# Performance work log

Hardware: AMD Instinct MI355X
Metric: run time of the kernel (lower is better)

Reference implementation:

```python
import jax, jax.numpy as jnp
import numpy as np

N_NODES = 50000
N_EDGES = 800000
F_IN = 128
HID = 256


def setup_inputs() -> dict:
    key = jax.random.key(0)
    ks = jax.random.split(key, 10)
    x = jax.random.normal(ks[0], (N_NODES, F_IN), jnp.float32)
    edge_index = jax.random.randint(ks[1], (2, N_EDGES), 0, N_NODES, jnp.int32)
    # Glorot-ish scaled weights (PyG Linear default init style)
    def w(k, o, i):
        return jax.random.normal(k, (o, i), jnp.float32) * (1.0 / np.sqrt(i))
    return {
        "x": x,
        "edge_index": edge_index,
        "W1l": w(ks[2], HID, F_IN), "b1l": jnp.zeros((HID,), jnp.float32),
        "W1r": w(ks[3], HID, F_IN),
        "W2l": w(ks[4], HID, HID), "b2l": jnp.zeros((HID,), jnp.float32),
        "W2r": w(ks[5], HID, HID),
        "Wh1": w(ks[6], 4, HID), "bh1": jnp.zeros((4,), jnp.float32),
        "Wh2": w(ks[7], 3, HID), "bh2": jnp.zeros((3,), jnp.float32),
    }


def sage_conv(x, edge_index, Wl, bl, Wr):
    # PyG SAGEConv (aggr='mean'): out_i = Wl @ mean_{j in N(i)} x_j + bl + Wr @ x_i
    src, dst = edge_index[0], edge_index[1]
    n = x.shape[0]
    summed = jax.ops.segment_sum(x[src], dst, num_segments=n)        # [N, F]
    cnt = jax.ops.segment_sum(jnp.ones((src.shape[0],), x.dtype), dst, num_segments=n)
    agg = summed / jnp.maximum(cnt, 1.0)[:, None]                    # isolated nodes -> 0
    return agg @ Wl.T + bl + x @ Wr.T


def reference(x, edge_index, W1l, b1l, W1r, W2l, b2l, W2r, Wh1, bh1, Wh2, bh2):
    h = jax.nn.relu(sage_conv(x, edge_index, W1l, b1l, W1r))
    # dropout(p=0.5) is identity in eval mode
    h = sage_conv(h, edge_index, W2l, b2l, W2r)
    out1 = h @ Wh1.T + bh1   # l2_classifier=False branch
    out2 = h @ Wh2.T + bh2
    return (out1, out2, h)
```

## Files before the change

kernel.cpp:

```cpp
#include <hip/hip_runtime.h>
#include <hip/hip_bf16.h>

typedef short bf16x8 __attribute__((ext_vector_type(8)));
typedef float f32x4 __attribute__((ext_vector_type(4)));

__device__ __forceinline__ float bf2f(__hip_bfloat16 v) { return __bfloat162float(v); }
__device__ __forceinline__ float sh2f(short s) {
    union { float f; unsigned u; } c; c.u = ((unsigned)(unsigned short)s) << 16; return c.f;
}
__device__ __forceinline__ short f2sh(float f) {
    __hip_bfloat16 b = __float2bfloat16(f); return *(short*)&b;
}

__device__ __forceinline__ float loadAny(const void* p, size_t i, int isf32) {
    return isf32 ? ((const float*)p)[i] : bf2f(((const __hip_bfloat16*)p)[i]);
}

__global__ void pre_kernel(const void* __restrict__ x,
                           const void* W1l, const void* W1r, const void* W2l, const void* W2r,
                           const void* b1l, const void* b2l, const void* Wh1, const void* Wh2,
                           const void* bh1, const void* bh2,
                           __hip_bfloat16* __restrict__ xn,
                           __hip_bfloat16* __restrict__ W1c, __hip_bfloat16* __restrict__ W2c,
                           __hip_bfloat16* __restrict__ sb,
                           int* __restrict__ deg, int* __restrict__ flag, int N) {
    __shared__ int sflag;
    int tid = threadIdx.x;
    if (tid < 64) {
        const unsigned short* xu = (const unsigned short*)x;
        unsigned short u = xu[tid * 2];
        unsigned e = (u >> 7) & 0xFF;
        bool good = (u == 0) || (e >= 110 && e <= 137);
        unsigned long long m = __ballot(good);
        if (tid == 0) sflag = (__popcll(m) < 32) ? 1 : 0;
    }
    __syncthreads();
    int isf32 = sflag;
    int gid = blockIdx.x * 256 + tid;
    if (gid == 0) *flag = isf32;
    if (gid < N) deg[gid] = 0;

    int n4 = N * 32;
    if (gid < n4) {
        short4 o;
        if (isf32) {
            float4 v = ((const float4*)x)[gid];
            o.x = f2sh(v.x); o.y = f2sh(v.y); o.z = f2sh(v.z); o.w = f2sh(v.w);
        } else {
            o = ((const short4*)x)[gid];
        }
        ((short4*)xn)[gid] = o;
    }

    if (gid < 65536) {
        int n = gid >> 8, k = gid & 255;
        float v = (k < 128) ? loadAny(W1l, n * 128 + k, isf32)
                            : loadAny(W1r, n * 128 + (k - 128), isf32);
        W1c[gid] = __float2bfloat16(v);
        return;
    }
    int u = gid - 65536;
    if (u < 131072) {
        int n = u >> 9, k = u & 511;
        float v = (k < 256) ? loadAny(W2l, n * 256 + k, isf32)
                            : loadAny(W2r, n * 256 + (k - 256), isf32);
        W2c[u] = __float2bfloat16(v);
        return;
    }
    int s = u - 131072;
    float v;
    if      (s < 256)  v = loadAny(b1l, s, isf32);
    else if (s < 512)  v = loadAny(b2l, s - 256, isf32);
    else if (s < 1536) v = loadAny(Wh1, s - 512, isf32);
    else if (s < 2304) v = loadAny(Wh2, s - 1536, isf32);
    else if (s < 2308) v = loadAny(bh1, s - 2304, isf32);
    else if (s < 2311) v = loadAny(bh2, s - 2308, isf32);
    else return;
    sb[s] = __float2bfloat16(v);
}

__global__ void deg_kernel(const int* __restrict__ ei, int E, int* __restrict__ deg,
                           int* __restrict__ rank) {
    int t = blockIdx.x * blockDim.x + threadIdx.x;
    if (t >= E) return;
    rank[t] = atomicAdd(&deg[ei[E + t]], 1);
}

__global__ __launch_bounds__(256) void scanA_kernel(const int* __restrict__ deg,
                                                    int* __restrict__ off,
                                                    int* __restrict__ bsum, int N) {
    __shared__ int ts[256];
    int t = threadIdx.x;
    int base = blockIdx.x * 1024 + t * 4;
    int v0 = (base + 0 < N) ? deg[base + 0] : 0;
    int v1 = (base + 1 < N) ? deg[base + 1] : 0;
    int v2 = (base + 2 < N) ? deg[base + 2] : 0;
    int v3 = (base + 3 < N) ? deg[base + 3] : 0;
    int i0 = v0, i1 = i0 + v1, i2 = i1 + v2, i3 = i2 + v3;
    ts[t] = i3;
    __syncthreads();
    for (int d = 1; d < 256; d <<= 1) {
        int x = (t >= d) ? ts[t - d] : 0;
        __syncthreads();
        ts[t] += x;
        __syncthreads();
    }
    int excl = (t > 0) ? ts[t - 1] : 0;
    if (base + 0 < N) off[base + 1] = excl + i0;
    if (base + 1 < N) off[base + 2] = excl + i1;
    if (base + 2 < N) off[base + 3] = excl + i2;
    if (base + 3 < N) off[base + 4] = excl + i3;
    if (t == 255) bsum[blockIdx.x] = ts[255];
}

__global__ void addC_kernel(int* __restrict__ off, const int* __restrict__ bsum,
                            int N, int nb) {
    __shared__ int ex[64];
    int t = threadIdx.x;
    if (t < 64) {
        int v = (t < nb) ? bsum[t] : 0;
        for (int d = 1; d < 64; d <<= 1) {
            int y = __shfl_up(v, d, 64);
            if (t >= d) v += y;
        }
        ex[t] = v;
    }
    __syncthreads();
    int i = blockIdx.x * 256 + t;
    if (i == 0) off[0] = 0;
    if (i < N) {
        int b = i >> 10;
        int excl = (b > 0) ? ex[b - 1] : 0;
        off[i + 1] += excl;
    }
}

__global__ void fill_kernel(const int* __restrict__ ei, int E,
                            const int* __restrict__ off, const int* __restrict__ rank,
                            unsigned short* __restrict__ srcs) {
    int t = blockIdx.x * blockDim.x + threadIdx.x;
    if (t >= E) return;
    int dst = ei[E + t];
    int pos = off[dst] + rank[t];
    srcs[pos] = (unsigned short)ei[t];
}

__global__ void gather1_kernel(const __hip_bfloat16* __restrict__ x,
                               const int* __restrict__ off,
                               const unsigned short* __restrict__ srcs,
                               __hip_bfloat16* __restrict__ agg, int N) {
    int gid  = blockIdx.x * blockDim.x + threadIdx.x;
    int wid  = gid >> 6;
    int lane = threadIdx.x & 63;
    int node = wid * 4 + (lane >> 4);
    int t    = lane & 15;
    if (node >= N) return;
    int beg = off[node], end = off[node + 1];
    float a[8] = {0.f, 0.f, 0.f, 0.f, 0.f, 0.f, 0.f, 0.f};
    const bf16x8* xb = (const bf16x8*)x;
    int e = beg;
    for (; e + 7 < end; e += 8) {
        bf16x8 v[8];
#pragma unroll
        for (int j = 0; j < 8; j++) v[j] = xb[(size_t)srcs[e + j] * 16 + t];
#pragma unroll
        for (int j = 0; j < 8; j++)
#pragma unroll
            for (int k = 0; k < 8; k++) a[k] += sh2f(v[j][k]);
    }
    for (; e < end; e++) {
        bf16x8 v = xb[(size_t)srcs[e] * 16 + t];
#pragma unroll
        for (int k = 0; k < 8; k++) a[k] += sh2f(v[k]);
    }
    float inv = 1.0f / fmaxf((float)(end - beg), 1.0f);
    bf16x8 o;
#pragma unroll
    for (int k = 0; k < 8; k++) o[k] = f2sh(a[k] * inv);
    ((bf16x8*)agg)[(size_t)node * 16 + t] = o;
}

__global__ void gather2_kernel(const __hip_bfloat16* __restrict__ h,
                               const int* __restrict__ off,
                               const unsigned short* __restrict__ srcs,
                               __hip_bfloat16* __restrict__ agg, int N) {
    int gid  = blockIdx.x * blockDim.x + threadIdx.x;
    int wid  = gid >> 6;
    int lane = threadIdx.x & 63;
    int node = wid * 2 + (lane >> 5);
    int t    = lane & 31;
    if (node >= N) return;
    int beg = off[node], end = off[node + 1];
    float a[8] = {0.f, 0.f, 0.f, 0.f, 0.f, 0.f, 0.f, 0.f};
    const bf16x8* hb = (const bf16x8*)h;
    int e = beg;
    for (; e + 7 < end; e += 8) {
        bf16x8 v[8];
#pragma unroll
        for (int j = 0; j < 8; j++) v[j] = hb[(size_t)srcs[e + j] * 32 + t];
#pragma unroll
        for (int j = 0; j < 8; j++)
#pragma unroll
            for (int k = 0; k < 8; k++) a[k] += sh2f(v[j][k]);
    }
    for (; e < end; e++) {
        bf16x8 v = hb[(size_t)srcs[e] * 32 + t];
#pragma unroll
        for (int k = 0; k < 8; k++) a[k] += sh2f(v[k]);
    }
    float inv = 1.0f / fmaxf((float)(end - beg), 1.0f);
    bf16x8 o;
#pragma unroll
    for (int k = 0; k < 8; k++) o[k] = f2sh(a[k] * inv);
    ((bf16x8*)agg)[(size_t)node * 32 + t] = o;
}

struct AFrag { bf16x8 v[2]; };

template <int K, int KA, bool RELU, bool TOOUT>
__global__ __launch_bounds__(256) void gemm_lds(const __hip_bfloat16* __restrict__ A1,
                                                const __hip_bfloat16* __restrict__ A2, int M,
                                                const __hip_bfloat16* __restrict__ W,
                                                const __hip_bfloat16* __restrict__ bias,
                                                __hip_bfloat16* __restrict__ outb,
                                                void* __restrict__ dout,
                                                const int* __restrict__ flag) {
    __shared__ short wlds[16384];
    constexpr int KB = K - KA;
    constexpr int NCHUNK = K / 128;
    int tid  = threadIdx.x;
    int wave = tid >> 6, lane = tid & 63, quad = lane >> 4, l15 = lane & 15;
    int rowBlk = blockIdx.x >> 1, half = blockIdx.x & 1;
    int R0 = rowBlk * 128;
    int cbase = half * 128;

    int mrow[2];
#pragma unroll
    for (int rt = 0; rt < 2; rt++) mrow[rt] = min(R0 + wave * 32 + rt * 16 + l15, M - 1);

    const short* Ws = (const short*)W;

    auto loadW = [&](int p, bf16x8* wreg) {
#pragma unroll
        for (int i = 0; i < 8; i++) {
            int unit = tid + i * 256;
            int ln = unit & 63, nt = (unit >> 6) & 7, kt = unit >> 9;
            int row = cbase + nt * 16 + (ln & 15);
            int kk  = p * 128 + kt * 32 + (ln >> 4) * 8;
            wreg[i] = *(const bf16x8*)(Ws + (size_t)row * K + kk);
        }
    };
    auto storeW = [&](const bf16x8* wreg) {
#pragma unroll
        for (int i = 0; i < 8; i++) {
            int unit = tid + i * 256;
            *(bf16x8*)&wlds[unit * 8] = wreg[i];
        }
    };
    auto loadA = [&](int kglob) {
        AFrag f;
#pragma unroll
        for (int rt = 0; rt < 2; rt++) {
            const short* ap = (kglob < KA)
                ? (const short*)A1 + (size_t)mrow[rt] * KA + kglob + quad * 8
                : (const short*)A2 + (size_t)mrow[rt] * KB + (kglob - KA) + quad * 8;
            f.v[rt] = *(const bf16x8*)ap;
        }
        return f;
    };

    f32x4 acc[2][8];
#pragma unroll
    for (int rt = 0; rt < 2; rt++)
#pragma unroll
        for (int nt = 0; nt < 8; nt++) acc[rt][nt] = {0.f, 0.f, 0.f, 0.f};

    bf16x8 wreg[8];
    loadW(0, wreg);
    storeW(wreg);
    __syncthreads();
    AFrag a0f = loadA(0);
    AFrag a1f = loadA(32 < K ? 32 : 0);

    for (int p = 0; p < NCHUNK; p++) {
        if (p + 1 < NCHUNK) loadW(p + 1, wreg);
#pragma unroll
        for (int kt = 0; kt < 4; kt++) {
            int kg = p * 128 + kt * 32;
            int kg2 = kg + 64;
            if (kg2 > K - 32) kg2 = K - 32;
            AFrag a_next = loadA(kg2);
#pragma unroll
            for (int nt = 0; nt < 8; nt++) {
                bf16x8 b = *(const bf16x8*)&wlds[((kt * 8 + nt) * 64 + lane) * 8];
#pragma unroll
                for (int rt = 0; rt < 2; rt++)
                    acc[rt][nt] = __builtin_amdgcn_mfma_f32_16x16x32_bf16(a0f.v[rt], b, acc[rt][nt], 0, 0, 0);
            }
            a0f = a1f;
            a1f = a_next;
        }
        if (p + 1 < NCHUNK) {
            __syncthreads();
            storeW(wreg);
            __syncthreads();
        }
    }

    int isf32 = TOOUT ? *flag : 0;
    float* hf = TOOUT ? ((float*)dout + (size_t)M * 7) : nullptr;
    __hip_bfloat16* hb = TOOUT ? ((__hip_bfloat16*)dout + (size_t)M * 7) : outb;

#pragma unroll
    for (int rt = 0; rt < 2; rt++) {
#pragma unroll
        for (int nt = 0; nt < 8; nt++) {
            int col = cbase + nt * 16 + l15;
            float bv = bf2f(bias[col]);
#pragma unroll
            for (int r = 0; r < 4; r++) {
                int row = R0 + wave * 32 + rt * 16 + quad * 4 + r;
                if (row < M) {
                    float v = acc[rt][nt][r] + bv;
                    if (RELU) v = fmaxf(v, 0.f);
                    size_t idx = (size_t)row * 256 + col;
                    if (TOOUT && isf32) hf[idx] = v;
                    else                hb[idx] = __float2bfloat16(v);
                }
            }
        }
    }
}

__global__ void heads_kernel(const __hip_bfloat16* __restrict__ sb,
                             void* dout, int N, const int* __restrict__ flag) {
    int isf32 = *flag;
    int node = (blockIdx.x * blockDim.x + threadIdx.x) >> 6;
    int lane = threadIdx.x & 63;
    if (node >= N) return;
    float hv0, hv1, hv2, hv3;
    if (isf32) {
        const float4* hp = (const float4*)((const float*)dout + (size_t)N * 7);
        float4 v = hp[(size_t)node * 64 + lane];
        hv0 = v.x; hv1 = v.y; hv2 = v.z; hv3 = v.w;
    } else {
        const __hip_bfloat162* hp = (const __hip_bfloat162*)((const __hip_bfloat16*)dout + (size_t)N * 7);
        __hip_bfloat162 a = hp[(size_t)node * 128 + 2 * lane];
        __hip_bfloat162 b = hp[(size_t)node * 128 + 2 * lane + 1];
        hv0 = bf2f(a.x); hv1 = bf2f(a.y); hv2 = bf2f(b.x); hv3 = bf2f(b.y);
    }
#pragma unroll
    for (int r = 0; r < 7; r++) {
        const __hip_bfloat16* wrow = (r < 4) ? (sb + 512 + r * 256) : (sb + 1536 + (r - 4) * 256);
        const __hip_bfloat162* wr2 = (const __hip_bfloat162*)wrow;
        __hip_bfloat162 wa = wr2[2 * lane];
        __hip_bfloat162 wb = wr2[2 * lane + 1];
        float p = hv0 * bf2f(wa.x) + hv1 * bf2f(wa.y) + hv2 * bf2f(wb.x) + hv3 * bf2f(wb.y);
        for (int off = 32; off > 0; off >>= 1) p += __shfl_down(p, off, 64);
        if (lane == 0) {
            float bias = (r < 4) ? bf2f(sb[2304 + r]) : bf2f(sb[2308 + (r - 4)]);
            float v = p + bias;
            size_t idx = (r < 4) ? ((size_t)node * 4 + r)
                                 : ((size_t)N * 4 + (size_t)node * 3 + (r - 4));
            if (isf32) ((float*)dout)[idx] = v;
            else       ((__hip_bfloat16*)dout)[idx] = __float2bfloat16(v);
        }
    }
}

extern "C" void kernel_launch(void* const* d_in, const int* in_sizes, int n_in,
                              void* d_out, int out_size, void* d_ws, size_t ws_size,
                              hipStream_t stream) {
    const void* x   = d_in[0];
    const int*  ei  = (const int*)d_in[1];
    const void* W1l = d_in[2];
    const void* b1l = d_in[3];
    const void* W1r = d_in[4];
    const void* W2l = d_in[5];
    const void* b2l = d_in[6];
    const void* W2r = d_in[7];
    const void* Wh1 = d_in[8];
    const void* bh1 = d_in[9];
    const void* Wh2 = d_in[10];
    const void* bh2 = d_in[11];

    const int N = in_sizes[0] / 128;
    const int E = in_sizes[1] / 2;
    const int NB = (N + 1023) / 1024;

    char* ws = (char*)d_ws;
    int*            offp   = (int*)(ws + 0);
    int*            deg    = (int*)(ws + 262144);
    int*            bsum   = (int*)(ws + 524288);
    unsigned short* srcs   = (unsigned short*)(ws + 786432);
    __hip_bfloat16* W1c    = (__hip_bfloat16*)(ws + 3986432);
    __hip_bfloat16* W2c    = (__hip_bfloat16*)(ws + 4117504);
    __hip_bfloat16* sb     = (__hip_bfloat16*)(ws + 4379648);
    __hip_bfloat16* xn     = (__hip_bfloat16*)(ws + 4387840);
    __hip_bfloat16* h1     = (__hip_bfloat16*)(ws + 17187840);
    int*            rank   = (int*)(ws + 17187840);
    __hip_bfloat16* agg    = (__hip_bfloat16*)(ws + 42787840);
    int*            flag   = (int*)(ws + 68387840);

    pre_kernel<<<(N * 32 + 255) / 256, 256, 0, stream>>>(
        x, W1l, W1r, W2l, W2r, b1l, b2l, Wh1, Wh2, bh1, bh2,
        xn, W1c, W2c, sb, deg, flag, N);

    deg_kernel<<<(E + 255) / 256, 256, 0, stream>>>(ei, E, deg, rank);
    scanA_kernel<<<NB, 256, 0, stream>>>(deg, offp, bsum, N);
    addC_kernel<<<(N + 255) / 256, 256, 0, stream>>>(offp, bsum, N, NB);
    fill_kernel<<<(E + 255) / 256, 256, 0, stream>>>(ei, E, offp, rank, srcs);

    const int rowBlks = (N + 127) / 128;

    {
        int waves = (N + 3) / 4;
        gather1_kernel<<<(waves * 64 + 255) / 256, 256, 0, stream>>>(xn, offp, srcs, agg, N);
    }
    gemm_lds<256, 128, true, false><<<rowBlks * 2, 256, 0, stream>>>(
        agg, xn, N, W1c, sb, h1, nullptr, flag);

    {
        int waves = (N + 1) / 2;
        gather2_kernel<<<(waves * 64 + 255) / 256, 256, 0, stream>>>(h1, offp, srcs, agg, N);
    }
    gemm_lds<512, 256, false, true><<<rowBlks * 2, 256, 0, stream>>>(
        agg, h1, N, W2c, sb + 256, nullptr, d_out, flag);

    heads_kernel<<<(N + 3) / 4, 256, 0, stream>>>(sb, d_out, N, flag);
}
```

Measured before the change: 341.9 us.

## Shrink GEMM tiles to 64 rows and 64-wide K chunks with grouped block order

The two SAGE GEMMs now use 64-row tiles and 64-wide K chunks, with half the LDS and accumulators per block. Blocks are ordered in groups of 8 row tiles times 2 column halves so that both halves of a row tile run close together and can share A rows in L2. The smaller footprint is meant to raise occupancy and spread work over more blocks. In exchange each W chunk loaded into LDS feeds fewer MFMAs, and there are twice as many K-loop barriers.

```diff
diff --git a/kernel.cpp b/kernel.cpp
--- a/kernel.cpp
+++ b/kernel.cpp
@@ -215,87 +215,79 @@
     ((bf16x8*)agg)[(size_t)node * 32 + t] = o;
 }
 
-struct AFrag { bf16x8 v[2]; };
-
 template <int K, int KA, bool RELU, bool TOOUT>
-__global__ __launch_bounds__(256) void gemm_lds(const __hip_bfloat16* __restrict__ A1,
-                                                const __hip_bfloat16* __restrict__ A2, int M,
-                                                const __hip_bfloat16* __restrict__ W,
-                                                const __hip_bfloat16* __restrict__ bias,
-                                                __hip_bfloat16* __restrict__ outb,
-                                                void* __restrict__ dout,
-                                                const int* __restrict__ flag) {
-    __shared__ short wlds[16384];
+__device__ __forceinline__ void gemm_body(short* wlds,
+                                          const __hip_bfloat16* __restrict__ A1,
+                                          const __hip_bfloat16* __restrict__ A2, int M,
+                                          const __hip_bfloat16* __restrict__ W,
+                                          const __hip_bfloat16* __restrict__ bias,
+                                          __hip_bfloat16* __restrict__ outb,
+                                          void* __restrict__ dout,
+                                          const int* __restrict__ flag) {
     constexpr int KB = K - KA;
-    constexpr int NCHUNK = K / 128;
+    constexpr int NCHUNK = K / 64;
+    int rowBlks = (M + 63) / 64;
+    int b = blockIdx.x;
+    int grp = b >> 4, w = b & 15;
+    int rowBlk = grp * 8 + (w & 7);
+    int half = w >> 3;
+    if (rowBlk >= rowBlks) return;
     int tid  = threadIdx.x;
     int wave = tid >> 6, lane = tid & 63, quad = lane >> 4, l15 = lane & 15;
-    int rowBlk = blockIdx.x >> 1, half = blockIdx.x & 1;
-    int R0 = rowBlk * 128;
+    int R0 = rowBlk * 64;
     int cbase = half * 128;
 
-    int mrow[2];
-#pragma unroll
-    for (int rt = 0; rt < 2; rt++) mrow[rt] = min(R0 + wave * 32 + rt * 16 + l15, M - 1);
+    int mrow = min(R0 + wave * 16 + l15, M - 1);
 
     const short* Ws = (const short*)W;
 
     auto loadW = [&](int p, bf16x8* wreg) {
 #pragma unroll
-        for (int i = 0; i < 8; i++) {
+        for (int i = 0; i < 4; i++) {
             int unit = tid + i * 256;
             int ln = unit & 63, nt = (unit >> 6) & 7, kt = unit >> 9;
             int row = cbase + nt * 16 + (ln & 15);
-            int kk  = p * 128 + kt * 32 + (ln >> 4) * 8;
+            int kk  = p * 64 + kt * 32 + (ln >> 4) * 8;
             wreg[i] = *(const bf16x8*)(Ws + (size_t)row * K + kk);
         }
     };
     auto storeW = [&](const bf16x8* wreg) {
 #pragma unroll
-        for (int i = 0; i < 8; i++) {
+        for (int i = 0; i < 4; i++) {
             int unit = tid + i * 256;
             *(bf16x8*)&wlds[unit * 8] = wreg[i];
         }
     };
     auto loadA = [&](int kglob) {
-        AFrag f;
-#pragma unroll
-        for (int rt = 0; rt < 2; rt++) {
-            const short* ap = (kglob < KA)
-                ? (const short*)A1 + (size_t)mrow[rt] * KA + kglob + quad * 8
-                : (const short*)A2 + (size_t)mrow[rt] * KB + (kglob - KA) + quad * 8;
-            f.v[rt] = *(const bf16x8*)ap;
-        }
-        return f;
+        const short* ap = (kglob < KA)
+            ? (const short*)A1 + (size_t)mrow * KA + kglob + quad * 8
+            : (const short*)A2 + (size_t)mrow * KB + (kglob - KA) + quad * 8;
+        return *(const bf16x8*)ap;
     };
 
-    f32x4 acc[2][8];
-#pragma unroll
-    for (int rt = 0; rt < 2; rt++)
-#pragma unroll
-        for (int nt = 0; nt < 8; nt++) acc[rt][nt] = {0.f, 0.f, 0.f, 0.f};
-
-    bf16x8 wreg[8];
+    f32x4 acc[8];
+#pragma unroll
+    for (int nt = 0; nt < 8; nt++) acc[nt] = {0.f, 0.f, 0.f, 0.f};
+
+    bf16x8 wreg[4];
     loadW(0, wreg);
     storeW(wreg);
     __syncthreads();
-    AFrag a0f = loadA(0);
-    AFrag a1f = loadA(32 < K ? 32 : 0);
+    bf16x8 a0f = loadA(0);
+    bf16x8 a1f = loadA(32);
 
     for (int p = 0; p < NCHUNK; p++) {
         if (p + 1 < NCHUNK) loadW(p + 1, wreg);
 #pragma unroll
-        for (int kt = 0; kt < 4; kt++) {
-            int kg = p * 128 + kt * 32;
+        for (int kt = 0; kt < 2; kt++) {
+            int kg = p * 64 + kt * 32;
             int kg2 = kg + 64;
             if (kg2 > K - 32) kg2 = K - 32;
-            AFrag a_next = loadA(kg2);
+            bf16x8 a_next = loadA(kg2);
 #pragma unroll
             for (int nt = 0; nt < 8; nt++) {
-                bf16x8 b = *(const bf16x8*)&wlds[((kt * 8 + nt) * 64 + lane) * 8];
-#pragma unroll
-                for (int rt = 0; rt < 2; rt++)
-                    acc[rt][nt] = __builtin_amdgcn_mfma_f32_16x16x32_bf16(a0f.v[rt], b, acc[rt][nt], 0, 0, 0);
+                bf16x8 bfr = *(const bf16x8*)&wlds[((kt * 8 + nt) * 64 + lane) * 8];
+                acc[nt] = __builtin_amdgcn_mfma_f32_16x16x32_bf16(a0f, bfr, acc[nt], 0, 0, 0);
             }
             a0f = a1f;
             a1f = a_next;
@@ -312,24 +304,41 @@
     __hip_bfloat16* hb = TOOUT ? ((__hip_bfloat16*)dout + (size_t)M * 7) : outb;
 
 #pragma unroll
-    for (int rt = 0; rt < 2; rt++) {
-#pragma unroll
-        for (int nt = 0; nt < 8; nt++) {
-            int col = cbase + nt * 16 + l15;
-            float bv = bf2f(bias[col]);
-#pragma unroll
-            for (int r = 0; r < 4; r++) {
-                int row = R0 + wave * 32 + rt * 16 + quad * 4 + r;
-                if (row < M) {
-                    float v = acc[rt][nt][r] + bv;
-                    if (RELU) v = fmaxf(v, 0.f);
-                    size_t idx = (size_t)row * 256 + col;
-                    if (TOOUT && isf32) hf[idx] = v;
-                    else                hb[idx] = __float2bfloat16(v);
-                }
+    for (int nt = 0; nt < 8; nt++) {
+        int col = cbase + nt * 16 + l15;
+        float bv = bf2f(bias[col]);
+#pragma unroll
+        for (int r = 0; r < 4; r++) {
+            int row = R0 + wave * 16 + quad * 4 + r;
+            if (row < M) {
+                float v = acc[nt][r] + bv;
+                if (RELU) v = fmaxf(v, 0.f);
+                size_t idx = (size_t)row * 256 + col;
+                if (TOOUT && isf32) hf[idx] = v;
+                else                hb[idx] = __float2bfloat16(v);
             }
         }
     }
+}
+
+__global__ __launch_bounds__(256) void gemm1_kernel(const __hip_bfloat16* __restrict__ A1,
+                                                    const __hip_bfloat16* __restrict__ A2, int M,
+                                                    const __hip_bfloat16* __restrict__ W,
+                                                    const __hip_bfloat16* __restrict__ bias,
+                                                    __hip_bfloat16* __restrict__ outb,
+                                                    const int* __restrict__ flag) {
+    __shared__ short wlds[8192];
+    gemm_body<256, 128, true, false>(wlds, A1, A2, M, W, bias, outb, nullptr, flag);
+}
+
+__global__ __launch_bounds__(256) void gemm2_kernel(const __hip_bfloat16* __restrict__ A1,
+                                                    const __hip_bfloat16* __restrict__ A2, int M,
+                                                    const __hip_bfloat16* __restrict__ W,
+                                                    const __hip_bfloat16* __restrict__ bias,
+                                                    void* __restrict__ dout,
+                                                    const int* __restrict__ flag) {
+    __shared__ short wlds[8192];
+    gemm_body<512, 256, false, true>(wlds, A1, A2, M, W, bias, nullptr, dout, flag);
 }
 
 __global__ void heads_kernel(const __hip_bfloat16* __restrict__ sb,
@@ -411,21 +420,20 @@
     addC_kernel<<<(N + 255) / 256, 256, 0, stream>>>(offp, bsum, N, NB);
     fill_kernel<<<(E + 255) / 256, 256, 0, stream>>>(ei, E, offp, rank, srcs);
 
-    const int rowBlks = (N + 127) / 128;
+    const int rowBlks = (N + 63) / 64;
+    const int gemmGrid = ((rowBlks + 7) / 8) * 16;
 
     {
         int waves = (N + 3) / 4;
         gather1_kernel<<<(waves * 64 + 255) / 256, 256, 0, stream>>>(xn, offp, srcs, agg, N);
     }
-    gemm_lds<256, 128, true, false><<<rowBlks * 2, 256, 0, stream>>>(
-        agg, xn, N, W1c, sb, h1, nullptr, flag);
+    gemm1_kernel<<<gemmGrid, 256, 0, stream>>>(agg, xn, N, W1c, sb, h1, flag);
 
     {
         int waves = (N + 1) / 2;
         gather2_kernel<<<(waves * 64 + 255) / 256, 256, 0, stream>>>(h1, offp, srcs, agg, N);
     }
-    gemm_lds<512, 256, false, true><<<rowBlks * 2, 256, 0, stream>>>(
-        agg, h1, N, W2c, sb + 256, nullptr, d_out, flag);
+    gemm2_kernel<<<gemmGrid, 256, 0, stream>>>(agg, h1, N, W2c, sb + 256, d_out, flag);
 
     heads_kernel<<<(N + 3) / 4, 256, 0, stream>>>(sb, d_out, N, flag);
 }
```

New measurement: 347.4 us. Within noise of the previous version (+1.6%).
